# Kernel optimization log

Measured on AMD Instinct MI355X. Metric: run time of the kernel, lower is better.

Reference implementation:

```python
import jax, jax.numpy as jnp
import numpy as np

K = 16            # neighbors per node
NB = 8            # number_of_basis
MAX_RADIUS = 10.0
MUL_1E = 32       # multiplicity of the 1e output block
DIM_0E = 64       # 64x0e block (structurally zero: no 1o x 0e -> 0e path)
DIM_2E = 80       # 16x2e block (structurally zero: no 1o x 0e -> 2e path)


def knn_edges(coords):
    """coords [B,N,3] -> (senders, receivers) flat int32 indices of length B*N*K.
    Edge (j -> i): j is one of the K nearest neighbors of i (self excluded),
    matching torch_geometric knn_graph(loop=False, flow=source_to_target)."""
    B, N, _ = coords.shape
    n2 = jnp.sum(coords * coords, -1)                       # [B,N]
    d2 = n2[:, :, None] + n2[:, None, :] - 2.0 * jnp.einsum('bnd,bmd->bnm', coords, coords)
    d2 = d2 + jnp.eye(N, dtype=coords.dtype) * 1e10         # exclude self-loops
    _, idx = jax.lax.top_k(-d2, K)                          # [B,N,K] neighbor ids per node
    offs = (jnp.arange(B) * N)[:, None, None]
    senders = (idx + offs).reshape(-1)
    receivers = (jnp.broadcast_to(jnp.arange(N)[None, :, None], (B, N, K)) + offs).reshape(-1)
    return senders, receivers


def gaussian_soft_one_hot(x, number):
    # x in [0,1], shape [E,1] -> [E,number]
    centers = jnp.linspace(0.0, 1.0, number).astype(x.dtype)
    sigma = 1.0 / number
    g = jnp.exp(-(x - centers) ** 2 / (2.0 * sigma * sigma))
    s = jnp.sum(g, -1, keepdims=True)
    s = jnp.where(s > 0, s, jnp.ones_like(s))
    return g / s


def setup_inputs():
    key = jax.random.key(0)
    ks = jax.random.split(key, 6)
    B, N = 8, 4096
    coords = jax.random.normal(ks[0], (B, N, 3), dtype=jnp.float32) * 10.0
    atom_types = jax.random.randint(ks[1], (B, N), 0, 20)
    residue_types = jax.random.randint(ks[2], (B, N), 0, 21)
    tp_weight = jax.random.normal(ks[3], (NB, MUL_1E), dtype=jnp.float32) / np.sqrt(NB)
    atom_emb = jax.random.normal(ks[4], (20, 112), dtype=jnp.float32).at[0].set(0.0)   # padding_idx=0
    res_emb = jax.random.normal(ks[5], (21, 112), dtype=jnp.float32).at[0].set(0.0)    # padding_idx=0
    return {"coords": coords, "atom_types": atom_types, "residue_types": residue_types,
            "tp_weight": tp_weight, "atom_emb": atom_emb, "res_emb": res_emb}


def reference(coords, atom_types, residue_types, tp_weight, atom_emb, res_emb):
    B, N, _ = coords.shape
    E = B * N * K
    senders, receivers = knn_edges(coords)
    cf = coords.reshape(-1, 3)
    r = cf[senders] - cf[receivers]                           # [E,3]
    dist = jnp.linalg.norm(r, axis=-1, keepdims=True)         # [E,1]
    r_hat = r / (dist + 1e-8)
    cutoff = jnp.clip(dist / MAX_RADIUS, 0.0, 1.0)
    rb = gaussian_soft_one_hot(cutoff, NB)                    # [E,NB]
    # FullyConnectedTensorProduct(1x1o/1e, NBx0e -> ... 32x1e ...):
    feat_1e = jnp.einsum('ev,vw,em->ewm', rb, tp_weight, r_hat) / np.sqrt(3.0)  # [E,32,3]
    # scatter_mean over receivers
    num = jax.ops.segment_sum(feat_1e.reshape(E, MUL_1E * 3), receivers, num_segments=B * N)
    cnt = jax.ops.segment_sum(jnp.ones((E,), coords.dtype), receivers, num_segments=B * N)
    agg_1e = (num / jnp.maximum(cnt, 1.0)[:, None]).reshape(B, N, MUL_1E * 3)
    zeros0 = jnp.zeros((B, N, DIM_0E), coords.dtype)
    zeros2 = jnp.zeros((B, N, DIM_2E), coords.dtype)
    pos_feats = jnp.concatenate([zeros0, agg_1e, zeros2], -1)  # [B,N,240]
    node_features = jnp.concatenate([pos_feats, atom_emb[atom_types], res_emb[residue_types]], -1)
    return node_features  # [B,N,464]
```

## Files before the change

### kernel.cpp

```cpp
#include <hip/hip_runtime.h>
#include <hip/hip_bf16.h>

#define NN    4096
#define KNEI  16
#define QPW   4
#define WPB   16
#define BLOCK (WPB * 64)
#define QPB   (WPB * QPW)
#define NEGB  -3.0e38f
#define PACKM 0xFFFFFFC0

typedef float f32x2 __attribute__((ext_vector_type(2)));
typedef int   i32x2 __attribute__((ext_vector_type(2)));

__device__ __forceinline__ int rlane(int v, int l)
{ return __builtin_amdgcn_readlane(v, l); }
__device__ __forceinline__ float rlanef(float v, int l)
{ return __int_as_float(__builtin_amdgcn_readlane(__float_as_int(v), l)); }

template<int CTRL>
__device__ __forceinline__ float rmax_step(float f)
{
    int s_ = __builtin_amdgcn_update_dpp(__float_as_int(f), __float_as_int(f),
                                         CTRL, 0xF, 0xF, false);
    return fmaxf(f, __int_as_float(s_));
}

template<int CTRL>
__device__ __forceinline__ void amax_step(float& f, int& i)
{
    int fs = __builtin_amdgcn_update_dpp(__float_as_int(f), __float_as_int(f),
                                         CTRL, 0xF, 0xF, false);
    int is = __builtin_amdgcn_update_dpp(i, i, CTRL, 0xF, 0xF, false);
    float ff = __int_as_float(fs);
    bool gt = ff > f;
    f = gt ? ff : f;
    i = gt ? is : i;
}

__device__ __forceinline__ void wave_amax(float f, int i, float& M, int& mi)
{
    amax_step<0x111>(f, i); amax_step<0x112>(f, i); amax_step<0x114>(f, i);
    amax_step<0x118>(f, i); amax_step<0x142>(f, i); amax_step<0x143>(f, i);
    M  = rlanef(f, 63);
    mi = rlane(i, 63);
}

__device__ __forceinline__ float row16_sum_dpp(float v)
{
    float f = v;
#define STEPA(CTRL)                                                          \
    { int s_ = __builtin_amdgcn_update_dpp(0, __float_as_int(f),             \
               (CTRL), 0xF, 0xF, true);                                      \
      f += __int_as_float(s_); }
    STEPA(0x111) STEPA(0x112) STEPA(0x114) STEPA(0x118)
#undef STEPA
    return f;
}

__device__ __forceinline__ float bpermf(int abyte, float v)
{ return __int_as_float(__builtin_amdgcn_ds_bpermute(abyte, __float_as_int(v))); }

__device__ __forceinline__ float sel4f(float a, float b, float c, float d, int q)
{
    float lo = (q & 1) ? b : a;
    float hi = (q & 1) ? d : c;
    return (q & 2) ? hi : lo;
}

#define SELFFIX(q, b, s)                                                     \
    {  int cb_ = __float_as_int(b) & 63;                                     \
       if ((((cb_) << 6) | (lane ^ cb_)) == q0 + (q)) { (b) = (s); (s) = NEGB; } \
       int cs_ = __float_as_int(s) & 63;                                     \
       if ((((cs_) << 6) | (lane ^ cs_)) == q0 + (q)) { (s) = NEGB; } }

#define REPLAY(qq, xq, yq, zq)                                               \
    {   int wq = __ffsll(ex & (0xFFFFull << ((qq) * 16))) - 1;               \
        int colq = rlane(col, wq);                                           \
        int kq   = rlane(kf,  wq);                                           \
        int j2 = (lane << 6) | (colq ^ lane);                                \
        float4 Pp = pts[j2];                                                 \
        float scr = fmaf(Pp.x,(xq), fmaf(Pp.y,(yq), fmaf(Pp.z,(zq), Pp.w))); \
        float sf = __int_as_float((__float_as_int(scr) & PACKM) | lane);     \
        if (j2 == q0 + (qq)) sf = NEGB;                                      \
        const int4* sp = (const int4*)&sel[wv * 64 + ((qq) << 4)];           \
        int4 sa = sp[0], sb = sp[1], sc = sp[2], sd = sp[3];                 \
        if (j2==sa.x || j2==sa.y || j2==sa.z || j2==sa.w) sf = NEGB;         \
        if (j2==sb.x || j2==sb.y || j2==sb.z || j2==sb.w) sf = NEGB;         \
        if (j2==sc.x || j2==sc.y || j2==sc.z || j2==sc.w) sf = NEGB;         \
        if (j2==sd.x || j2==sd.y || j2==sd.z || j2==sd.w) sf = NEGB;         \
        float M1; int i1;                                                    \
        wave_amax(sf, j2, M1, i1);                                           \
        float sf2 = (j2 == i1) ? NEGB : sf;                                  \
        float M2; int i2;                                                    \
        wave_amax(sf2, j2, M2, i2);                                          \
        bool ow = (lane == (qq) * 16 + (colq & 15));                         \
        if (kq == 0)      { pb0 = ow ? M1 : pb0; ps0 = ow ? M2 : ps0; }      \
        else if (kq == 1) { pb1 = ow ? M1 : pb1; ps1 = ow ? M2 : ps1; }      \
        else if (kq == 2) { pb2 = ow ? M1 : pb2; ps2 = ow ? M2 : ps2; }      \
        else              { pb3 = ow ? M1 : pb3; ps3 = ow ? M2 : ps3; }      \
    }

__global__ __launch_bounds__(BLOCK, 8)
void protein_enc_kernel(const float* __restrict__ coords,
                        const int*   __restrict__ atypes,
                        const int*   __restrict__ rtypes,
                        const float* __restrict__ tpw,
                        const float* __restrict__ aemb,
                        const float* __restrict__ remb,
                        float* __restrict__ out)
{
    __shared__ float4 pts[NN];
    __shared__ float  sW[8 * 32];
    __shared__ int    sel[WPB * 64];

    const int tid  = threadIdx.x;
    const int lane = tid & 63;
    const int wv   = tid >> 6;
    const int bpb  = NN / QPB;
    const int batch    = blockIdx.x / bpb;
    const int nodeBase = (blockIdx.x % bpb) * QPB;

    const float* cb = coords + (size_t)batch * NN * 3;

    for (int p = tid; p < NN; p += BLOCK) {
        float x = cb[3*p], y = cb[3*p+1], z = cb[3*p+2];
        pts[p] = make_float4(x, y, z, -0.5f * (x*x + y*y + z*z));
    }
    if (tid < 256) sW[tid] = tpw[tid];
    sel[wv * 64 + lane] = -1;
    __syncthreads();

    const int q0 = nodeBase + wv * QPW;
    const float4 P0 = pts[q0],   P1 = pts[q0+1];
    const float4 P2 = pts[q0+2], P3 = pts[q0+3];
    const float x0 = P0.x, y0 = P0.y, z0 = P0.z;
    const float x1 = P1.x, y1 = P1.y, z1 = P1.z;
    const float x2 = P2.x, y2 = P2.y, z2 = P2.z;
    const float x3 = P3.x, y3 = P3.y, z3 = P3.z;

    const f32x2 qAx = {x0, x1}, qAy = {y0, y1}, qAz = {z0, z1};
    const f32x2 qBx = {x2, x3}, qBy = {y2, y3}, qBz = {z2, z3};
    const i32x2 M2v = {(int)PACKM, (int)PACKM};

    f32x2 bA = {NEGB, NEGB}, sA = {NEGB, NEGB};
    f32x2 bB = {NEGB, NEGB}, sB = {NEGB, NEGB};

    #pragma unroll 8
    for (int c = 0; c < NN / 64; ++c) {
        int j = (c << 6) | (lane ^ c);
        float4 P = pts[j];
        f32x2 vx = {P.x, P.x}, vy = {P.y, P.y}, vz = {P.z, P.z}, vw = {P.w, P.w};
        f32x2 dA = __builtin_elementwise_fma(vx, qAx,
                   __builtin_elementwise_fma(vy, qAy,
                   __builtin_elementwise_fma(vz, qAz, vw)));
        f32x2 dB = __builtin_elementwise_fma(vx, qBx,
                   __builtin_elementwise_fma(vy, qBy,
                   __builtin_elementwise_fma(vz, qBz, vw)));
        i32x2 cc = {c, c};
        f32x2 pA = __builtin_bit_cast(f32x2,
                     (__builtin_bit_cast(i32x2, dA) & M2v) | cc);
        f32x2 pB = __builtin_bit_cast(f32x2,
                     (__builtin_bit_cast(i32x2, dB) & M2v) | cc);
        sA = __builtin_elementwise_max(sA, __builtin_elementwise_min(pA, bA));
        bA = __builtin_elementwise_max(bA, pA);
        sB = __builtin_elementwise_max(sB, __builtin_elementwise_min(pB, bB));
        bB = __builtin_elementwise_max(bB, pB);
    }

    float b0 = bA.x, b1 = bA.y, b2 = bB.x, b3 = bB.y;
    float s0 = sA.x, s1 = sA.y, s2 = sB.x, s3 = sB.y;

    SELFFIX(0, b0, s0)
    SELFFIX(1, b1, s1)
    SELFFIX(2, b2, s2)
    SELFFIX(3, b3, s3)

    const int q  = lane >> 4;
    const int gt = lane & 15;
    float pb0, pb1, pb2, pb3, ps0, ps1, ps2, ps3;
    {
        const int ab = gt << 2;
#define PULL(K, PB, PS)                                                      \
        {   int a = ab + ((K) << 6);                                         \
            PB = sel4f(bpermf(a,b0), bpermf(a,b1), bpermf(a,b2), bpermf(a,b3), q); \
            PS = sel4f(bpermf(a,s0), bpermf(a,s1), bpermf(a,s2), bpermf(a,s3), q); \
        }
        PULL(0, pb0, ps0)
        PULL(1, pb1, ps1)
        PULL(2, pb2, ps2)
        PULL(3, pb3, ps3)
#undef PULL
    }

    const unsigned long long gmask = 0xFFFFull << (q << 4);
    const int selbase = wv * 64 + (q << 4);

    #pragma unroll 1
    for (int r = 0; r < KNEI; ++r) {
        float f = fmaxf(fmaxf(pb0, pb1), fmaxf(pb2, pb3));
        f = rmax_step<0x121>(f); f = rmax_step<0x122>(f);
        f = rmax_step<0x124>(f); f = rmax_step<0x128>(f);
        bool c0 = (pb0 == f), c1 = (pb1 == f), c2 = (pb2 == f), c3 = (pb3 == f);
        unsigned long long m = __ballot(c0 | c1 | c2 | c3);
        int w = __ffsll(m & gmask) - 1;
        bool iwin = (lane == w);
        int kf = c0 ? 0 : (c1 ? 1 : (c2 ? 2 : 3));
        bool o0 = iwin && c0;
        bool o1 = iwin && !c0 && c1;
        bool o2 = iwin && !c0 && !c1 && c2;
        bool o3 = iwin && !c0 && !c1 && !c2;
        int cw  = __float_as_int(f) & 63;
        int col = gt + (kf << 4);
        int jw  = (cw << 6) | (col ^ cw);
        if (iwin) sel[selbase + r] = jw;
        float pskf = o1 ? ps1 : (o2 ? ps2 : (o3 ? ps3 : ps0));
        bool e = iwin && (pskf == NEGB);
        pb0 = o0 ? ps0 : pb0;  ps0 = o0 ? NEGB : ps0;
        pb1 = o1 ? ps1 : pb1;  ps1 = o1 ? NEGB : ps1;
        pb2 = o2 ? ps2 : pb2;  ps2 = o2 ? NEGB : ps2;
        pb3 = o3 ? ps3 : pb3;  ps3 = o3 ? NEGB : ps3;
        unsigned long long ex = __ballot(e);
        if (ex) {
            if ((ex >>  0) & 0xFFFFull) REPLAY(0, x0, y0, z0)
            if ((ex >> 16) & 0xFFFFull) REPLAY(1, x1, y1, z1)
            if ((ex >> 32) & 0xFFFFull) REPLAY(2, x2, y2, z2)
            if ((ex >> 48) & 0xFFFFull) REPLAY(3, x3, y3, z3)
        }
    }

    int selIdx = sel[wv * 64 + lane];

    float xq = (q & 2) ? ((q & 1) ? x3 : x2) : ((q & 1) ? x1 : x0);
    float yq = (q & 2) ? ((q & 1) ? y3 : y2) : ((q & 1) ? y1 : y0);
    float zq = (q & 2) ? ((q & 1) ? z3 : z2) : ((q & 1) ? z1 : z0);

    float4 P = pts[selIdx];
    float rx = P.x - xq, ry = P.y - yq, rz = P.z - zq;
    float dist = sqrtf(rx*rx + ry*ry + rz*rz);
    float inv  = 1.0f / (dist + 1e-8f);
    float hx = rx * inv, hy = ry * inv, hz = rz * inv;
    float cu = fminf(dist / 10.0f, 1.0f);
    float A = expf(cu * cu * -32.0f);
    float E = expf(cu * (64.0f / 7.0f));
    const float K[8] = {1.0f, 0.5204501f, 0.0733697f, 0.00280164f,
                        2.897772e-05f, 8.11857e-08f, 6.16130e-11f,
                        1.2664166e-14f};
    float gg[8];
    float t = A, ssum = A;
    gg[0] = A;
    #pragma unroll
    for (int v = 1; v < 8; ++v) { t *= E; gg[v] = t * K[v]; ssum += gg[v]; }
    float is = 1.0f / ssum;
    float S[24];
    #pragma unroll
    for (int v = 0; v < 8; ++v) {
        float rbv = gg[v] * is;
        S[3*v]   = rbv * hx;
        S[3*v+1] = rbv * hy;
        S[3*v+2] = rbv * hz;
    }
    #pragma unroll
    for (int t2 = 0; t2 < 24; ++t2) S[t2] = row16_sum_dpp(S[t2]);

    float wcol[8];
    #pragma unroll
    for (int v = 0; v < 8; ++v) wcol[v] = sW[32*v + (lane & 31)];

    const float scale = 0.036084391824351613f;
    const float4 z4 = make_float4(0.f, 0.f, 0.f, 0.f);

    #pragma unroll
    for (int qq = 0; qq < QPW; ++qq) {
        const int gq = batch * NN + q0 + qq;
        float sg[24];
        #pragma unroll
        for (int t2 = 0; t2 < 24; ++t2) sg[t2] = rlanef(S[t2], 16 * qq + 15);

        float* onode = out + (size_t)gq * 464;
        float4* o4 = (float4*)onode;
        if (lane < 16)       o4[lane] = z4;
        else if (lane < 36)  o4[lane + 24] = z4;

        if (lane < 32) {
            float a0 = 0.f, a1 = 0.f, a2 = 0.f;
            #pragma unroll
            for (int v = 0; v < 8; ++v) {
                a0 = fmaf(wcol[v], sg[3*v],   a0);
                a1 = fmaf(wcol[v], sg[3*v+1], a1);
                a2 = fmaf(wcol[v], sg[3*v+2], a2);
            }
            onode[64 + 3*lane]     = a0 * scale;
            onode[64 + 3*lane + 1] = a1 * scale;
            onode[64 + 3*lane + 2] = a2 * scale;
        }

        const int at = atypes[gq];
        const int rt = rtypes[gq];
        if (lane < 56) {
            float4 v = (lane < 28)
                ? ((const float4*)(aemb + 112*at))[lane]
                : ((const float4*)(remb + 112*rt))[lane - 28];
            o4[60 + lane] = v;
        }
    }
}

extern "C" void kernel_launch(void* const* d_in, const int* in_sizes, int n_in,
                              void* d_out, int out_size, void* d_ws, size_t ws_size,
                              hipStream_t stream)
{
    const float* coords = (const float*)d_in[0];
    const int*   at     = (const int*)  d_in[1];
    const int*   rt     = (const int*)  d_in[2];
    const float* tpw    = (const float*)d_in[3];
    const float* ae     = (const float*)d_in[4];
    const float* re     = (const float*)d_in[5];
    float* out = (float*)d_out;

    const int B = in_sizes[1] / NN;
    dim3 grid(B * (NN / QPB));
    protein_enc_kernel<<<grid, BLOCK, 0, stream>>>(coords, at, rt, tpw, ae, re, out);
}
```

Before: 73.71 us.

## Sort points by x and restrict kNN scan to a local window with fallback

A new pre-pass sorts each batch's points by x-coordinate with a bitonic sort. It writes sorted float4 points and their original ids to the workspace. The main kernel then scans only a 1088-point window around each query block instead of all 4096 points. A distance-bound check triggers a full-scan fallback when the window may miss true neighbours, and outputs are written to the original node ids. Block size is halved to 8 waves. This cuts most of the brute-force distance work, but adds a separate single-block-per-batch sort kernel and divergent fallback scans.

```diff
diff --git a/kernel.cpp b/kernel.cpp
--- a/kernel.cpp
+++ b/kernel.cpp
@@ -4,9 +4,11 @@
 #define NN    4096
 #define KNEI  16
 #define QPW   4
-#define WPB   16
+#define WPB   8
 #define BLOCK (WPB * 64)
 #define QPB   (WPB * QPW)
+#define WIN   1088
+#define NCHF  17
 #define NEGB  -3.0e38f
 #define PACKM 0xFFFFFFC0
 
@@ -68,77 +70,19 @@
     return (q & 2) ? hi : lo;
 }
 
-#define SELFFIX(q, b, s)                                                     \
-    {  int cb_ = __float_as_int(b) & 63;                                     \
-       if ((((cb_) << 6) | (lane ^ cb_)) == q0 + (q)) { (b) = (s); (s) = NEGB; } \
-       int cs_ = __float_as_int(s) & 63;                                     \
-       if ((((cs_) << 6) | (lane ^ cs_)) == q0 + (q)) { (s) = NEGB; } }
-
-#define REPLAY(qq, xq, yq, zq)                                               \
-    {   int wq = __ffsll(ex & (0xFFFFull << ((qq) * 16))) - 1;               \
-        int colq = rlane(col, wq);                                           \
-        int kq   = rlane(kf,  wq);                                           \
-        int j2 = (lane << 6) | (colq ^ lane);                                \
-        float4 Pp = pts[j2];                                                 \
-        float scr = fmaf(Pp.x,(xq), fmaf(Pp.y,(yq), fmaf(Pp.z,(zq), Pp.w))); \
-        float sf = __int_as_float((__float_as_int(scr) & PACKM) | lane);     \
-        if (j2 == q0 + (qq)) sf = NEGB;                                      \
-        const int4* sp = (const int4*)&sel[wv * 64 + ((qq) << 4)];           \
-        int4 sa = sp[0], sb = sp[1], sc = sp[2], sd = sp[3];                 \
-        if (j2==sa.x || j2==sa.y || j2==sa.z || j2==sa.w) sf = NEGB;         \
-        if (j2==sb.x || j2==sb.y || j2==sb.z || j2==sb.w) sf = NEGB;         \
-        if (j2==sc.x || j2==sc.y || j2==sc.z || j2==sc.w) sf = NEGB;         \
-        if (j2==sd.x || j2==sd.y || j2==sd.z || j2==sd.w) sf = NEGB;         \
-        float M1; int i1;                                                    \
-        wave_amax(sf, j2, M1, i1);                                           \
-        float sf2 = (j2 == i1) ? NEGB : sf;                                  \
-        float M2; int i2;                                                    \
-        wave_amax(sf2, j2, M2, i2);                                          \
-        bool ow = (lane == (qq) * 16 + (colq & 15));                         \
-        if (kq == 0)      { pb0 = ow ? M1 : pb0; ps0 = ow ? M2 : ps0; }      \
-        else if (kq == 1) { pb1 = ow ? M1 : pb1; ps1 = ow ? M2 : ps1; }      \
-        else if (kq == 2) { pb2 = ow ? M1 : pb2; ps2 = ow ? M2 : ps2; }      \
-        else              { pb3 = ow ? M1 : pb3; ps3 = ow ? M2 : ps3; }      \
-    }
-
-__global__ __launch_bounds__(BLOCK, 8)
-void protein_enc_kernel(const float* __restrict__ coords,
-                        const int*   __restrict__ atypes,
-                        const int*   __restrict__ rtypes,
-                        const float* __restrict__ tpw,
-                        const float* __restrict__ aemb,
-                        const float* __restrict__ remb,
-                        float* __restrict__ out)
-{
-    __shared__ float4 pts[NN];
-    __shared__ float  sW[8 * 32];
-    __shared__ int    sel[WPB * 64];
-
-    const int tid  = threadIdx.x;
-    const int lane = tid & 63;
-    const int wv   = tid >> 6;
-    const int bpb  = NN / QPB;
-    const int batch    = blockIdx.x / bpb;
-    const int nodeBase = (blockIdx.x % bpb) * QPB;
-
-    const float* cb = coords + (size_t)batch * NN * 3;
-
-    for (int p = tid; p < NN; p += BLOCK) {
-        float x = cb[3*p], y = cb[3*p+1], z = cb[3*p+2];
-        pts[p] = make_float4(x, y, z, -0.5f * (x*x + y*y + z*z));
-    }
-    if (tid < 256) sW[tid] = tpw[tid];
-    sel[wv * 64 + lane] = -1;
-    __syncthreads();
-
-    const int q0 = nodeBase + wv * QPW;
-    const float4 P0 = pts[q0],   P1 = pts[q0+1];
-    const float4 P2 = pts[q0+2], P3 = pts[q0+3];
-    const float x0 = P0.x, y0 = P0.y, z0 = P0.z;
-    const float x1 = P1.x, y1 = P1.y, z1 = P1.z;
-    const float x2 = P2.x, y2 = P2.y, z2 = P2.z;
-    const float x3 = P3.x, y3 = P3.y, z3 = P3.z;
-
+#define SELFFIX(bq, sq_, soff)                                               \
+    {  int cb_ = __float_as_int(bq) & 63;                                    \
+       if ((((cb_) << 6) | (lane ^ cb_)) == (soff)) { (bq) = (sq_); (sq_) = NEGB; } \
+       int cs_ = __float_as_int(sq_) & 63;                                   \
+       if ((((cs_) << 6) | (lane ^ cs_)) == (soff)) { (sq_) = NEGB; } }
+
+template<int NCH>
+__device__ __forceinline__ void knn_scan(
+    const float4* __restrict__ src, int base, int rq0,
+    float x0, float y0, float z0, float x1, float y1, float z1,
+    float x2, float y2, float z2, float x3, float y3, float z3,
+    int lane, int q, int gt, int* __restrict__ selw, float& f15)
+{
     const f32x2 qAx = {x0, x1}, qAy = {y0, y1}, qAz = {z0, z1};
     const f32x2 qBx = {x2, x3}, qBy = {y2, y3}, qBz = {z2, z3};
     const i32x2 M2v = {(int)PACKM, (int)PACKM};
@@ -146,10 +90,10 @@
     f32x2 bA = {NEGB, NEGB}, sA = {NEGB, NEGB};
     f32x2 bB = {NEGB, NEGB}, sB = {NEGB, NEGB};
 
-    #pragma unroll 8
-    for (int c = 0; c < NN / 64; ++c) {
-        int j = (c << 6) | (lane ^ c);
-        float4 P = pts[j];
+    #pragma unroll
+    for (int c = 0; c < NCH; ++c) {
+        int off = (c << 6) | (lane ^ c);
+        float4 P = src[off];
         f32x2 vx = {P.x, P.x}, vy = {P.y, P.y}, vz = {P.z, P.z}, vw = {P.w, P.w};
         f32x2 dA = __builtin_elementwise_fma(vx, qAx,
                    __builtin_elementwise_fma(vy, qAy,
@@ -171,13 +115,12 @@
     float b0 = bA.x, b1 = bA.y, b2 = bB.x, b3 = bB.y;
     float s0 = sA.x, s1 = sA.y, s2 = sB.x, s3 = sB.y;
 
-    SELFFIX(0, b0, s0)
-    SELFFIX(1, b1, s1)
-    SELFFIX(2, b2, s2)
-    SELFFIX(3, b3, s3)
-
-    const int q  = lane >> 4;
-    const int gt = lane & 15;
+    const int sq0 = rq0 - base;
+    SELFFIX(b0, s0, sq0)
+    SELFFIX(b1, s1, sq0 + 1)
+    SELFFIX(b2, s2, sq0 + 2)
+    SELFFIX(b3, s3, sq0 + 3)
+
     float pb0, pb1, pb2, pb3, ps0, ps1, ps2, ps3;
     {
         const int ab = gt << 2;
@@ -193,9 +136,38 @@
 #undef PULL
     }
 
+#define REPLAY(qq, xq, yq, zq)                                               \
+    {   int wq = __ffsll(ex & (0xFFFFull << ((qq) * 16))) - 1;               \
+        int colq = rlane(col, wq);                                           \
+        int kq   = rlane(kf,  wq);                                           \
+        float sf = NEGB;                                                     \
+        int off2 = (lane << 6) | (colq ^ lane);                              \
+        if (lane < NCH) {                                                    \
+            float4 Pp = src[off2];                                           \
+            float scr = fmaf(Pp.x,(xq), fmaf(Pp.y,(yq), fmaf(Pp.z,(zq), Pp.w))); \
+            sf = __int_as_float((__float_as_int(scr) & PACKM) | lane);       \
+            int j2 = base + off2;                                            \
+            if (j2 == rq0 + (qq)) sf = NEGB;                                 \
+            const int4* sp = (const int4*)&selw[(qq) << 4];                  \
+            int4 sa = sp[0], sb = sp[1], sc = sp[2], sd = sp[3];             \
+            if (j2==sa.x || j2==sa.y || j2==sa.z || j2==sa.w) sf = NEGB;     \
+            if (j2==sb.x || j2==sb.y || j2==sb.z || j2==sb.w) sf = NEGB;     \
+            if (j2==sc.x || j2==sc.y || j2==sc.z || j2==sc.w) sf = NEGB;     \
+            if (j2==sd.x || j2==sd.y || j2==sd.z || j2==sd.w) sf = NEGB;     \
+        }                                                                    \
+        float M1; int i1;                                                    \
+        wave_amax(sf, lane, M1, i1);                                         \
+        float sf2 = (lane == i1) ? NEGB : sf;                                \
+        float M2; int i2;                                                    \
+        wave_amax(sf2, lane, M2, i2);                                        \
+        bool ow = (lane == (qq) * 16 + (colq & 15));                         \
+        if (kq == 0)      { pb0 = ow ? M1 : pb0; ps0 = ow ? M2 : ps0; }      \
+        else if (kq == 1) { pb1 = ow ? M1 : pb1; ps1 = ow ? M2 : ps1; }      \
+        else if (kq == 2) { pb2 = ow ? M1 : pb2; ps2 = ow ? M2 : ps2; }      \
+        else              { pb3 = ow ? M1 : pb3; ps3 = ow ? M2 : ps3; }      \
+    }
+
     const unsigned long long gmask = 0xFFFFull << (q << 4);
-    const int selbase = wv * 64 + (q << 4);
-
     #pragma unroll 1
     for (int r = 0; r < KNEI; ++r) {
         float f = fmaxf(fmaxf(pb0, pb1), fmaxf(pb2, pb3));
@@ -212,8 +184,9 @@
         bool o3 = iwin && !c0 && !c1 && !c2;
         int cw  = __float_as_int(f) & 63;
         int col = gt + (kf << 4);
-        int jw  = (cw << 6) | (col ^ cw);
-        if (iwin) sel[selbase + r] = jw;
+        int jw  = base + ((cw << 6) | (col ^ cw));
+        if (iwin) selw[(q << 4) + r] = jw;
+        if (r == KNEI - 1) f15 = f;
         float pskf = o1 ? ps1 : (o2 ? ps2 : (o3 ? ps3 : ps0));
         bool e = iwin && (pskf == NEGB);
         pb0 = o0 ? ps0 : pb0;  ps0 = o0 ? NEGB : ps0;
@@ -228,14 +201,116 @@
             if ((ex >> 48) & 0xFFFFull) REPLAY(3, x3, y3, z3)
         }
     }
-
-    int selIdx = sel[wv * 64 + lane];
+#undef REPLAY
+}
+
+__global__ __launch_bounds__(1024)
+void sort_kernel(const float* __restrict__ coords,
+                 float4* __restrict__ spts, int* __restrict__ sids)
+{
+    __shared__ float kx[NN];
+    __shared__ int   ki[NN];
+    const int b = blockIdx.x;
+    const int t = threadIdx.x;
+    const float* cb = coords + (size_t)b * NN * 3;
+    for (int i = t; i < NN; i += 1024) { kx[i] = cb[3*i]; ki[i] = i; }
+    __syncthreads();
+    for (int k = 2; k <= NN; k <<= 1) {
+        for (int j = k >> 1; j > 0; j >>= 1) {
+            for (int i = t; i < NN; i += 1024) {
+                int ixj = i ^ j;
+                if (ixj > i) {
+                    bool up = ((i & k) == 0);
+                    float xa = kx[i], xb = kx[ixj];
+                    int   ia = ki[i], ib = ki[ixj];
+                    bool sw = up ? (xa > xb || (xa == xb && ia > ib))
+                                 : (xa < xb || (xa == xb && ia < ib));
+                    if (sw) { kx[i]=xb; kx[ixj]=xa; ki[i]=ib; ki[ixj]=ia; }
+                }
+            }
+            __syncthreads();
+        }
+    }
+    for (int r = t; r < NN; r += 1024) {
+        int id = ki[r];
+        float x = cb[3*id], y = cb[3*id+1], z = cb[3*id+2];
+        spts[(size_t)b*NN + r] = make_float4(x, y, z, -0.5f*(x*x + y*y + z*z));
+        sids[(size_t)b*NN + r] = id;
+    }
+}
+
+__global__ __launch_bounds__(BLOCK, 8)
+void protein_enc_kernel(const float4* __restrict__ spts,
+                        const int*   __restrict__ sids,
+                        const int*   __restrict__ atypes,
+                        const int*   __restrict__ rtypes,
+                        const float* __restrict__ tpw,
+                        const float* __restrict__ aemb,
+                        const float* __restrict__ remb,
+                        float* __restrict__ out)
+{
+    __shared__ float4 win[WIN];
+    __shared__ float  sW[8 * 32];
+    __shared__ int    sel[WPB * 64];
+
+    const int tid  = threadIdx.x;
+    const int lane = tid & 63;
+    const int wv   = tid >> 6;
+    const int bpb  = NN / QPB;
+    const int batch    = blockIdx.x / bpb;
+    const int nodeBase = (blockIdx.x % bpb) * QPB;
+
+    const float4* gsb = spts + (size_t)batch * NN;
+
+    int blo = nodeBase - 528;
+    if (blo < 0) blo = 0;
+    blo &= ~63;
+    if (blo > NN - WIN) blo = NN - WIN;
+
+    for (int t = tid; t < WIN; t += BLOCK) win[t] = gsb[blo + t];
+    if (tid < 256) sW[tid] = tpw[tid];
+    sel[tid] = -1;
+    __syncthreads();
+
+    const int rq0 = nodeBase + wv * QPW;
+    const float4 Q0 = win[rq0 - blo],   Q1 = win[rq0+1 - blo];
+    const float4 Q2 = win[rq0+2 - blo], Q3 = win[rq0+3 - blo];
+    const float x0 = Q0.x, y0 = Q0.y, z0 = Q0.z;
+    const float x1 = Q1.x, y1 = Q1.y, z1 = Q1.z;
+    const float x2 = Q2.x, y2 = Q2.y, z2 = Q2.z;
+    const float x3 = Q3.x, y3 = Q3.y, z3 = Q3.z;
+
+    const int q  = lane >> 4;
+    const int gt = lane & 15;
+    int* selw = &sel[wv * 64];
+
+    float f15 = NEGB;
+    knn_scan<NCHF>(win, blo, rq0, x0,y0,z0, x1,y1,z1, x2,y2,z2, x3,y3,z3,
+                   lane, q, gt, selw, f15);
 
     float xq = (q & 2) ? ((q & 1) ? x3 : x2) : ((q & 1) ? x1 : x0);
     float yq = (q & 2) ? ((q & 1) ? y3 : y2) : ((q & 1) ? y1 : y0);
     float zq = (q & 2) ? ((q & 1) ? z3 : z2) : ((q & 1) ? z1 : z0);
 
-    float4 P = pts[selIdx];
+    {
+        float n2q = xq*xq + yq*yq + zq*zq;
+        float d2safe = fmaf(-2.0f, f15, n2q) + 0.125f;
+        float xlo = win[0].x, xhi = win[WIN-1].x;
+        bool lok = (blo == 0) ||
+                   ((xq - xlo) * (xq - xlo) >= d2safe);
+        bool rok = (blo + WIN >= NN) ||
+                   ((xhi - xq) * (xhi - xq) >= d2safe);
+        unsigned long long fb = __ballot(!(lok && rok));
+        if (fb) {
+            selw[lane] = -1;
+            float fd;
+            knn_scan<64>(gsb, 0, rq0, x0,y0,z0, x1,y1,z1, x2,y2,z2, x3,y3,z3,
+                         lane, q, gt, selw, fd);
+        }
+    }
+
+    int selIdx = selw[lane];
+    float4 P = gsb[selIdx];
     float rx = P.x - xq, ry = P.y - yq, rz = P.z - zq;
     float dist = sqrtf(rx*rx + ry*ry + rz*rz);
     float inv  = 1.0f / (dist + 1e-8f);
@@ -272,7 +347,8 @@
 
     #pragma unroll
     for (int qq = 0; qq < QPW; ++qq) {
-        const int gq = batch * NN + q0 + qq;
+        const int gid = sids[(size_t)batch * NN + rq0 + qq];
+        const int gq  = batch * NN + gid;
         float sg[24];
         #pragma unroll
         for (int t2 = 0; t2 < 24; ++t2) sg[t2] = rlanef(S[t2], 16 * qq + 15);
@@ -319,6 +395,10 @@
     float* out = (float*)d_out;
 
     const int B = in_sizes[1] / NN;
-    dim3 grid(B * (NN / QPB));
-    protein_enc_kernel<<<grid, BLOCK, 0, stream>>>(coords, at, rt, tpw, ae, re, out);
-}
+    float4* spts = (float4*)d_ws;
+    int*    sids = (int*)((char*)d_ws + (size_t)B * NN * sizeof(float4));
+
+    sort_kernel<<<B, 1024, 0, stream>>>(coords, spts, sids);
+    protein_enc_kernel<<<B * (NN / QPB), BLOCK, 0, stream>>>(
+        spts, sids, at, rt, tpw, ae, re, out);
+}
```

Result: slower. 218.8 us (+196.8%).

## Precompute packed points in a prep kernel and read them from global memory

Applied to the files above, without the earlier changes.

A separate prep kernel now builds the packed float4 points (xyz plus -0.5|p|^2) in workspace. The main kernel reads them straight from global memory/L1 instead of staging all 4096 points into LDS per block, and it drops the __syncthreads. Block size shrinks from 16 to 4 waves, so the grid has four times as many blocks. The aim is to remove the redundant per-block LDS fill, which was repeated for every 64-query block. The cost is that the hot brute-force scan loop now issues global/L1 loads instead of LDS reads, and there is an extra kernel launch.

```diff
diff --git a/kernel.cpp b/kernel.cpp
--- a/kernel.cpp
+++ b/kernel.cpp
@@ -4,7 +4,7 @@
 #define NN    4096
 #define KNEI  16
 #define QPW   4
-#define WPB   16
+#define WPB   4
 #define BLOCK (WPB * 64)
 #define QPB   (WPB * QPW)
 #define NEGB  -3.0e38f
@@ -79,7 +79,7 @@
         int colq = rlane(col, wq);                                           \
         int kq   = rlane(kf,  wq);                                           \
         int j2 = (lane << 6) | (colq ^ lane);                                \
-        float4 Pp = pts[j2];                                                 \
+        float4 Pp = gsb[j2];                                                 \
         float scr = fmaf(Pp.x,(xq), fmaf(Pp.y,(yq), fmaf(Pp.z,(zq), Pp.w))); \
         float sf = __int_as_float((__float_as_int(scr) & PACKM) | lane);     \
         if (j2 == q0 + (qq)) sf = NEGB;                                      \
@@ -101,8 +101,19 @@
         else              { pb3 = ow ? M1 : pb3; ps3 = ow ? M2 : ps3; }      \
     }
 
+__global__ __launch_bounds__(256)
+void prep_kernel(const float* __restrict__ coords, float4* __restrict__ spts,
+                 int total)
+{
+    int i = blockIdx.x * 256 + threadIdx.x;
+    if (i < total) {
+        float x = coords[3*i], y = coords[3*i+1], z = coords[3*i+2];
+        spts[i] = make_float4(x, y, z, -0.5f * (x*x + y*y + z*z));
+    }
+}
+
 __global__ __launch_bounds__(BLOCK, 8)
-void protein_enc_kernel(const float* __restrict__ coords,
+void protein_enc_kernel(const float4* __restrict__ spts,
                         const int*   __restrict__ atypes,
                         const int*   __restrict__ rtypes,
                         const float* __restrict__ tpw,
@@ -110,9 +121,7 @@
                         const float* __restrict__ remb,
                         float* __restrict__ out)
 {
-    __shared__ float4 pts[NN];
-    __shared__ float  sW[8 * 32];
-    __shared__ int    sel[WPB * 64];
+    __shared__ int sel[WPB * 64];
 
     const int tid  = threadIdx.x;
     const int lane = tid & 63;
@@ -121,19 +130,12 @@
     const int batch    = blockIdx.x / bpb;
     const int nodeBase = (blockIdx.x % bpb) * QPB;
 
-    const float* cb = coords + (size_t)batch * NN * 3;
-
-    for (int p = tid; p < NN; p += BLOCK) {
-        float x = cb[3*p], y = cb[3*p+1], z = cb[3*p+2];
-        pts[p] = make_float4(x, y, z, -0.5f * (x*x + y*y + z*z));
-    }
-    if (tid < 256) sW[tid] = tpw[tid];
+    const float4* gsb = spts + (size_t)batch * NN;
     sel[wv * 64 + lane] = -1;
-    __syncthreads();
 
     const int q0 = nodeBase + wv * QPW;
-    const float4 P0 = pts[q0],   P1 = pts[q0+1];
-    const float4 P2 = pts[q0+2], P3 = pts[q0+3];
+    const float4 P0 = gsb[q0],   P1 = gsb[q0+1];
+    const float4 P2 = gsb[q0+2], P3 = gsb[q0+3];
     const float x0 = P0.x, y0 = P0.y, z0 = P0.z;
     const float x1 = P1.x, y1 = P1.y, z1 = P1.z;
     const float x2 = P2.x, y2 = P2.y, z2 = P2.z;
@@ -149,7 +151,7 @@
     #pragma unroll 8
     for (int c = 0; c < NN / 64; ++c) {
         int j = (c << 6) | (lane ^ c);
-        float4 P = pts[j];
+        float4 P = gsb[j];
         f32x2 vx = {P.x, P.x}, vy = {P.y, P.y}, vz = {P.z, P.z}, vw = {P.w, P.w};
         f32x2 dA = __builtin_elementwise_fma(vx, qAx,
                    __builtin_elementwise_fma(vy, qAy,
@@ -235,7 +237,7 @@
     float yq = (q & 2) ? ((q & 1) ? y3 : y2) : ((q & 1) ? y1 : y0);
     float zq = (q & 2) ? ((q & 1) ? z3 : z2) : ((q & 1) ? z1 : z0);
 
-    float4 P = pts[selIdx];
+    float4 P = gsb[selIdx];
     float rx = P.x - xq, ry = P.y - yq, rz = P.z - zq;
     float dist = sqrtf(rx*rx + ry*ry + rz*rz);
     float inv  = 1.0f / (dist + 1e-8f);
@@ -265,7 +267,7 @@
 
     float wcol[8];
     #pragma unroll
-    for (int v = 0; v < 8; ++v) wcol[v] = sW[32*v + (lane & 31)];
+    for (int v = 0; v < 8; ++v) wcol[v] = tpw[32*v + (lane & 31)];
 
     const float scale = 0.036084391824351613f;
     const float4 z4 = make_float4(0.f, 0.f, 0.f, 0.f);
@@ -319,6 +321,10 @@
     float* out = (float*)d_out;
 
     const int B = in_sizes[1] / NN;
-    dim3 grid(B * (NN / QPB));
-    protein_enc_kernel<<<grid, BLOCK, 0, stream>>>(coords, at, rt, tpw, ae, re, out);
-}
+    const int total = B * NN;
+    float4* spts = (float4*)d_ws;
+
+    prep_kernel<<<(total + 255) / 256, 256, 0, stream>>>(coords, spts, total);
+    protein_enc_kernel<<<B * (NN / QPB), BLOCK, 0, stream>>>(
+        spts, at, rt, tpw, ae, re, out);
+}
```

Result: slower. 83.51 us (+13.3%).
